# Kernel optimization log

Hardware: AMD Instinct MI355X
Metric: run time of the kernel (lower is better)

The kernel has to match this reference:

```python
import jax, jax.numpy as jnp
import numpy as np

CHUNK = 32
PRIOR = 64
POSE = 512
PRED = 128
B = 2048


def setup_inputs() -> dict:
    key = jax.random.key(0)
    k1, k2, k3, k4, k5, k6 = jax.random.split(key, 6)
    initial_feature = jax.random.normal(k1, (B, PRIOR, POSE), dtype=jnp.float32)
    pred_feature = jax.random.normal(k2, (B, PRED, POSE), dtype=jnp.float32)
    s1 = 1.0 / np.sqrt(CHUNK * POSE)
    s2 = 1.0 / np.sqrt(POSE)
    W1 = jax.random.uniform(k3, (POSE, CHUNK * POSE), minval=-s1, maxval=s1, dtype=jnp.float32)
    b1 = jax.random.uniform(k4, (POSE,), minval=-s1, maxval=s1, dtype=jnp.float32)
    W2 = jax.random.uniform(k5, (POSE, POSE), minval=-s2, maxval=s2, dtype=jnp.float32)
    b2 = jax.random.uniform(k6, (POSE,), minval=-s2, maxval=s2, dtype=jnp.float32)
    return {"initial_feature": initial_feature, "pred_feature": pred_feature,
            "W1": W1, "b1": b1, "W2": W2, "b2": b2}


def reference(initial_feature, pred_feature, W1, b1, W2, b2):
    Bn = initial_feature.shape[0]
    # last CHUNK prior frames flattened -> [B, CHUNK*POSE]
    x = initial_feature[:, PRIOR - CHUNK:, :].reshape(Bn, -1)
    # spatial_chunk_encoder (Dropout is identity in eval mode)
    mem = (x @ W1.T + b1) @ W2.T + b2          # [B, POSE]
    head = pred_feature[:, :CHUNK, :]          # [B, CHUNK, POSE]
    score = jnp.einsum('bd,bcd->bc', mem, head)  # per-token dot product
    g = jax.nn.sigmoid(score)[..., None]       # [B, CHUNK, 1]
    blended = g * head + (1.0 - g) * mem[:, None, :]
    return pred_feature.at[:, :CHUNK, :].set(blended)
```

## Files before the change

kernel.cpp:

```cpp
#include <hip/hip_runtime.h>
#include <hip/hip_bf16.h>
#include <stdint.h>

#define CHUNKC 32
#define PRIORC 64
#define POSEC 512
#define PREDC 128
#define NB 2048
#define K1 (CHUNKC*POSEC)

typedef __attribute__((ext_vector_type(8))) short bf16x8;
typedef __attribute__((ext_vector_type(4))) float f32x4;
typedef __attribute__((ext_vector_type(4))) float f4v;
typedef __attribute__((ext_vector_type(4))) unsigned short u16x4;

__device__ __forceinline__ unsigned short f2b(float f) {
    union { float f; unsigned int u; } x; x.f = f;
    unsigned int r = x.u + 0x7fffu + ((x.u >> 16) & 1u);
    return (unsigned short)(r >> 16);
}

__device__ __forceinline__ void gload_lds16(const void* g, void* l) {
    __builtin_amdgcn_global_load_lds(
        (const __attribute__((address_space(1))) unsigned int*)g,
        (__attribute__((address_space(3))) unsigned int*)l, 16, 0, 0);
}

#define XN4   8388608
#define W1N4  2097152
#define W2N4  65536
__global__ __launch_bounds__(256) void cvt_all_kernel(const f4v* __restrict__ init,
                                                      const f4v* __restrict__ W1,
                                                      const f4v* __restrict__ W2,
                                                      u16x4* __restrict__ xb,
                                                      u16x4* __restrict__ w1b,
                                                      u16x4* __restrict__ w2b) {
    const int64_t n = XN4 + W1N4 + W2N4;
    const int64_t stride = (int64_t)gridDim.x * blockDim.x;
    for (int64_t i = (int64_t)blockIdx.x * blockDim.x + threadIdx.x; i < n; i += stride) {
        f4v v; u16x4* dst;
        if (i < XN4) {
            int64_t b = i >> 12, r = i & 4095;
            v = __builtin_nontemporal_load(init + b * 8192 + 4096 + r);
            dst = xb + i;
        } else if (i < XN4 + W1N4) {
            v = __builtin_nontemporal_load(W1 + (i - XN4));
            dst = w1b + (i - XN4);
        } else {
            v = __builtin_nontemporal_load(W2 + (i - XN4 - W1N4));
            dst = w2b + (i - XN4 - W1N4);
        }
        u16x4 o;
        o[0] = f2b(v[0]); o[1] = f2b(v[1]); o[2] = f2b(v[2]); o[3] = f2b(v[3]);
        __builtin_nontemporal_store(o, dst);
    }
}

template<int KSv>
__global__ __launch_bounds__(512) void gemm1_kernel(const ushort* __restrict__ xb,
                                                    const ushort* __restrict__ w1b,
                                                    float* __restrict__ part) {
    __shared__ ushort As[256][64];
    __shared__ ushort Bs[256][64];
    const int t = threadIdx.x;
    const int l = t & 63, wid = t >> 6;
    const int wr = wid >> 2, wc = wid & 3;
    const int cpx = (16 * KSv) >> 3;
    const int orig = (blockIdx.x & 7) * cpx + (blockIdx.x >> 3);
    const int mt = orig & 7, nt = (orig >> 3) & 1, ks = orig >> 4;
    const int KCHv = K1 / KSv;

    f32x4 acc[8][4] = {};

    const ushort* aG = xb  + (int64_t)(mt * 256) * K1 + ks * KCHv;
    const ushort* bG = w1b + (int64_t)(nt * 256) * K1 + ks * KCHv;
    const int srow = t >> 3, scol = (t & 7) * 8;

    const int fr = l & 15, fq = l >> 4;

    for (int k0 = 0; k0 < KCHv; k0 += 64) {
#pragma unroll
        for (int i = 0; i < 4; ++i) {
            gload_lds16(aG + (int64_t)(i * 64 + srow) * K1 + k0 + scol,
                        (char*)&As[0][0] + i * 8192 + wid * 1024);
            gload_lds16(bG + (int64_t)(i * 64 + srow) * K1 + k0 + scol,
                        (char*)&Bs[0][0] + i * 8192 + wid * 1024);
        }
        __syncthreads();
#pragma unroll
        for (int k2 = 0; k2 < 2; ++k2) {
            bf16x8 a[8], b[4];
#pragma unroll
            for (int m = 0; m < 8; ++m)
                a[m] = *(const bf16x8*)&As[wr * 128 + m * 16 + fr][k2 * 32 + fq * 8];
#pragma unroll
            for (int n = 0; n < 4; ++n)
                b[n] = *(const bf16x8*)&Bs[wc * 64 + n * 16 + fr][k2 * 32 + fq * 8];
#pragma unroll
            for (int m = 0; m < 8; ++m)
#pragma unroll
                for (int n = 0; n < 4; ++n)
                    acc[m][n] = __builtin_amdgcn_mfma_f32_16x16x32_bf16(a[m], b[n], acc[m][n], 0, 0, 0);
        }
        __syncthreads();
    }

    float* P = part + (int64_t)ks * NB * POSEC;
    const int mbase = mt * 256 + wr * 128, nbase = nt * 256 + wc * 64;
#pragma unroll
    for (int m = 0; m < 8; ++m)
#pragma unroll
        for (int n = 0; n < 4; ++n) {
            int row0 = mbase + m * 16 + fq * 4;
            int col  = nbase + n * 16 + fr;
#pragma unroll
            for (int r = 0; r < 4; ++r)
                P[(int64_t)(row0 + r) * POSEC + col] = acc[m][n][r];
        }
}

template<int KSv>
__global__ __launch_bounds__(256) void reduce_kernel(const float4* __restrict__ part,
                                                     const float* __restrict__ b1,
                                                     ushort4* __restrict__ A2) {
    const int i4 = blockIdx.x * 256 + threadIdx.x;
    float4 s = part[i4];
#pragma unroll
    for (int k = 1; k < KSv; ++k) {
        float4 p = part[(int64_t)k * 262144 + i4];
        s.x += p.x; s.y += p.y; s.z += p.z; s.w += p.w;
    }
    const int col = (i4 * 4) & 511;
    float4 bv = *(const float4*)&b1[col];
    A2[i4] = make_ushort4(f2b(s.x + bv.x), f2b(s.y + bv.y), f2b(s.z + bv.z), f2b(s.w + bv.w));
}

__global__ __launch_bounds__(256) void gemm2_kernel(const ushort* __restrict__ A2,
                                                    const ushort* __restrict__ w2b,
                                                    const float* __restrict__ b2,
                                                    float* __restrict__ mem) {
    __shared__ ushort As[64][64];
    __shared__ ushort Bs[64][64];
    const int t = threadIdx.x;
    const int l = t & 63, wid = t >> 6;
    const int wr = wid >> 1, wc = wid & 1;
    const int mt = blockIdx.x >> 3, nt = blockIdx.x & 7;

    f32x4 acc[2][2] = {};
    const ushort* aG = A2  + (int64_t)(mt * 64) * POSEC;
    const ushort* bG = w2b + (int64_t)(nt * 64) * POSEC;
    const int srow = t >> 3, scol = (t & 7) * 8;
    const int fr = l & 15, fq = l >> 4;

    for (int k0 = 0; k0 < POSEC; k0 += 64) {
#pragma unroll
        for (int i = 0; i < 2; ++i) {
            gload_lds16(aG + (int64_t)(i * 32 + srow) * POSEC + k0 + scol,
                        (char*)&As[0][0] + i * 4096 + wid * 1024);
            gload_lds16(bG + (int64_t)(i * 32 + srow) * POSEC + k0 + scol,
                        (char*)&Bs[0][0] + i * 4096 + wid * 1024);
        }
        __syncthreads();
#pragma unroll
        for (int k2 = 0; k2 < 2; ++k2) {
            bf16x8 a[2], b[2];
#pragma unroll
            for (int m = 0; m < 2; ++m)
                a[m] = *(const bf16x8*)&As[wr * 32 + m * 16 + fr][k2 * 32 + fq * 8];
#pragma unroll
            for (int n = 0; n < 2; ++n)
                b[n] = *(const bf16x8*)&Bs[wc * 32 + n * 16 + fr][k2 * 32 + fq * 8];
#pragma unroll
            for (int m = 0; m < 2; ++m)
#pragma unroll
                for (int n = 0; n < 2; ++n)
                    acc[m][n] = __builtin_amdgcn_mfma_f32_16x16x32_bf16(a[m], b[n], acc[m][n], 0, 0, 0);
        }
        __syncthreads();
    }

    const int mbase = mt * 64 + wr * 32, nbase = nt * 64 + wc * 32;
#pragma unroll
    for (int m = 0; m < 2; ++m)
#pragma unroll
        for (int n = 0; n < 2; ++n) {
            int row0 = mbase + m * 16 + fq * 4;
            int col  = nbase + n * 16 + fr;
            float bias = b2[col];
#pragma unroll
            for (int r = 0; r < 4; ++r)
                mem[(int64_t)(row0 + r) * POSEC + col] = acc[m][n][r] + bias;
        }
}

__global__ __launch_bounds__(256) void blend_kernel(const float* __restrict__ pred,
                                                    const float* __restrict__ mem,
                                                    float* __restrict__ out) {
    const int b = blockIdx.x;
    const int t = threadIdx.x;
    __shared__ float sm[POSEC];
    __shared__ float sg[CHUNKC];

    sm[t]       = mem[(int64_t)b * POSEC + t];
    sm[t + 256] = mem[(int64_t)b * POSEC + 256 + t];
    __syncthreads();

    const int l = t & 63, wid = t >> 6;
    const float4* sm4 = (const float4*)sm;
    const float4* p4 = (const float4*)pred + (int64_t)b * 16384;
    float4* o4 = (float4*)out + (int64_t)b * 16384;

#pragma unroll
    for (int ci = 0; ci < 8; ++ci) {
        int c = wid * 8 + ci;
        float4 h0 = p4[c * 128 + l * 2];
        float4 h1 = p4[c * 128 + l * 2 + 1];
        float4 m0 = sm4[l * 2];
        float4 m1 = sm4[l * 2 + 1];
        float s = h0.x * m0.x + h0.y * m0.y + h0.z * m0.z + h0.w * m0.w
                + h1.x * m1.x + h1.y * m1.y + h1.z * m1.z + h1.w * m1.w;
#pragma unroll
        for (int o = 32; o; o >>= 1) s += __shfl_xor(s, o);
        if (l == 0) sg[c] = 1.0f / (1.0f + expf(-s));
    }
    __syncthreads();

#pragma unroll
    for (int i = 0; i < 16; ++i) {
        int idx = i * 256 + t;
        int row = idx >> 7, c4 = idx & 127;
        float g = sg[row];
        float4 h = p4[idx];
        float4 m = sm4[c4];
        float4 r;
        r.x = g * h.x + (1.0f - g) * m.x;
        r.y = g * h.y + (1.0f - g) * m.y;
        r.z = g * h.z + (1.0f - g) * m.z;
        r.w = g * h.w + (1.0f - g) * m.w;
        o4[idx] = r;
    }
#pragma unroll
    for (int i = 0; i < 48; ++i) {
        int idx = 4096 + i * 256 + t;
        f4v h = __builtin_nontemporal_load((const f4v*)p4 + idx);
        __builtin_nontemporal_store(h, (f4v*)o4 + idx);
    }
}


extern "C" void kernel_launch(void* const* d_in, const int* in_sizes, int n_in,
                              void* d_out, int out_size, void* d_ws, size_t ws_size,
                              hipStream_t stream) {
    const float* init = (const float*)d_in[0];
    const float* pred = (const float*)d_in[1];
    const float* W1   = (const float*)d_in[2];
    const float* b1   = (const float*)d_in[3];
    const float* W2   = (const float*)d_in[4];
    const float* b2   = (const float*)d_in[5];
    float* out = (float*)d_out;

    const int KS = (ws_size >= 157810688u) ? 16 : 8;

    char* ws = (char*)d_ws;
    ushort* xb   = (ushort*)(ws);
    ushort* w1b  = (ushort*)(ws + 67108864);
    ushort* w2b  = (ushort*)(ws + 83886080);
    float*  part = (float*) (ws + 84410368);
    char*   after = ws + 84410368 + (size_t)KS * 4194304;
    ushort* A2   = (ushort*)(after);
    float*  mem  = (float*) (after + 2097152);

    cvt_all_kernel<<<2560, 256, 0, stream>>>((const f4v*)init, (const f4v*)W1,
                                             (const f4v*)W2,
                                             (u16x4*)xb, (u16x4*)w1b, (u16x4*)w2b);
    if (KS == 16) {
        gemm1_kernel<16><<<256, 512, 0, stream>>>(xb, w1b, part);
        reduce_kernel<16><<<1024, 256, 0, stream>>>((const float4*)part, b1, (ushort4*)A2);
    } else {
        gemm1_kernel<8><<<128, 512, 0, stream>>>(xb, w1b, part);
        reduce_kernel<8><<<1024, 256, 0, stream>>>((const float4*)part, b1, (ushort4*)A2);
    }
    gemm2_kernel<<<256, 256, 0, stream>>>(A2, w2b, b2, mem);
    blend_kernel<<<NB, 256, 0, stream>>>(pred, mem, out);
}
```

Before: 333.9 us.

## Overlap pred tail copy with GEMM1 by adding copy blocks to its grid

```diff
diff --git a/kernel.cpp b/kernel.cpp
--- a/kernel.cpp
+++ b/kernel.cpp
@@ -8,6 +8,7 @@
 #define PREDC 128
 #define NB 2048
 #define K1 (CHUNKC*POSEC)
+#define NCOPY 768
 
 typedef __attribute__((ext_vector_type(8))) short bf16x8;
 typedef __attribute__((ext_vector_type(4))) float f32x4;
@@ -57,15 +58,34 @@
 }
 
 template<int KSv>
-__global__ __launch_bounds__(512) void gemm1_kernel(const ushort* __restrict__ xb,
-                                                    const ushort* __restrict__ w1b,
-                                                    float* __restrict__ part) {
+__global__ __launch_bounds__(512) void gemm1_copy_kernel(const ushort* __restrict__ xb,
+                                                         const ushort* __restrict__ w1b,
+                                                         float* __restrict__ part,
+                                                         const f4v* __restrict__ pred4,
+                                                         f4v* __restrict__ out4) {
     __shared__ ushort As[256][64];
     __shared__ ushort Bs[256][64];
+    const int NG = 16 * KSv;
     const int t = threadIdx.x;
+
+    if ((int)blockIdx.x >= NG) {
+        const int cid = blockIdx.x - NG;
+        int64_t j0 = (int64_t)cid * 512 + t;
+        int b0 = (int)(j0 / 12288);
+        int rem = (int)(j0 - (int64_t)b0 * 12288);
+        int64_t idx = (int64_t)b0 * 16384 + 4096 + rem;
+#pragma unroll 4
+        for (int it = 0; it < 64; ++it) {
+            f4v h = __builtin_nontemporal_load(pred4 + idx);
+            __builtin_nontemporal_store(h, out4 + idx);
+            idx += 524288;
+        }
+        return;
+    }
+
     const int l = t & 63, wid = t >> 6;
     const int wr = wid >> 2, wc = wid & 3;
-    const int cpx = (16 * KSv) >> 3;
+    const int cpx = NG >> 3;
     const int orig = (blockIdx.x & 7) * cpx + (blockIdx.x >> 3);
     const int mt = orig & 7, nt = (orig >> 3) & 1, ks = orig >> 4;
     const int KCHv = K1 / KSv;
@@ -193,9 +213,9 @@
         }
 }
 
-__global__ __launch_bounds__(256) void blend_kernel(const float* __restrict__ pred,
-                                                    const float* __restrict__ mem,
-                                                    float* __restrict__ out) {
+__global__ __launch_bounds__(256) void blend_head_kernel(const float* __restrict__ pred,
+                                                         const float* __restrict__ mem,
+                                                         float* __restrict__ out) {
     const int b = blockIdx.x;
     const int t = threadIdx.x;
     __shared__ float sm[POSEC];
@@ -239,12 +259,6 @@
         r.w = g * h.w + (1.0f - g) * m.w;
         o4[idx] = r;
     }
-#pragma unroll
-    for (int i = 0; i < 48; ++i) {
-        int idx = 4096 + i * 256 + t;
-        f4v h = __builtin_nontemporal_load((const f4v*)p4 + idx);
-        __builtin_nontemporal_store(h, (f4v*)o4 + idx);
-    }
 }
 
 
@@ -274,12 +288,14 @@
                                              (const f4v*)W2,
                                              (u16x4*)xb, (u16x4*)w1b, (u16x4*)w2b);
     if (KS == 16) {
-        gemm1_kernel<16><<<256, 512, 0, stream>>>(xb, w1b, part);
+        gemm1_copy_kernel<16><<<256 + NCOPY, 512, 0, stream>>>(xb, w1b, part,
+                                                               (const f4v*)pred, (f4v*)out);
         reduce_kernel<16><<<1024, 256, 0, stream>>>((const float4*)part, b1, (ushort4*)A2);
     } else {
-        gemm1_kernel<8><<<128, 512, 0, stream>>>(xb, w1b, part);
+        gemm1_copy_kernel<8><<<128 + NCOPY, 512, 0, stream>>>(xb, w1b, part,
+                                                              (const f4v*)pred, (f4v*)out);
         reduce_kernel<8><<<1024, 256, 0, stream>>>((const float4*)part, b1, (ushort4*)A2);
     }
     gemm2_kernel<<<256, 256, 0, stream>>>(A2, w2b, b2, mem);
-    blend_kernel<<<NB, 256, 0, stream>>>(pred, mem, out);
-}
+    blend_head_kernel<<<NB, 256, 0, stream>>>(pred, mem, out);
+}
```

New measurement: 378.3 us. 13.3% more time.
